# Kernel optimization log

Hardware: AMD Instinct MI355X
Metric: run time of the kernel (lower is better)

Reference implementation:

```python
import jax, jax.numpy as jnp
import numpy as np

B, T, C, H = 4, 1024, 512, 8
HD = C // H
N_NODE, F_DIM, TOTAL_DIM = 64, 8, 16
SCALE = 1.0 / np.sqrt(HD)


def _build_mask():
    # causal tril with every (total_dim-1 mod total_dim)-th COLUMN zeroed
    m = np.tril(np.ones((T, T), dtype=np.float32))
    m[:, TOTAL_DIM - 1::TOTAL_DIM] = 0.0
    return jnp.asarray(m)

MASK = _build_mask()  # (T, T), 1 = keep, 0 = mask


def setup_inputs() -> dict:
    key = jax.random.key(0)
    ks = jax.random.split(key, 12)
    s = 0.02
    return {
        "x": jax.random.normal(ks[0], (B, T, C), dtype=jnp.float32),
        "attn_bias": jax.random.normal(ks[1], (H, N_NODE, N_NODE), dtype=jnp.float32) * 0.1,
        "Wq": jax.random.normal(ks[2], (C, C), dtype=jnp.float32) * s,
        "bq": jax.random.normal(ks[3], (C,), dtype=jnp.float32) * s,
        "Wk": jax.random.normal(ks[4], (C, C), dtype=jnp.float32) * s,
        "bk": jax.random.normal(ks[5], (C,), dtype=jnp.float32) * s,
        "Wv": jax.random.normal(ks[6], (C, C), dtype=jnp.float32) * s,
        "bv": jax.random.normal(ks[7], (C,), dtype=jnp.float32) * s,
        "Wp": jax.random.normal(ks[8], (C, C), dtype=jnp.float32) * s,
        "bp": jax.random.normal(ks[9], (C,), dtype=jnp.float32) * s,
    }


def reference(x, attn_bias, Wq, bq, Wk, bk, Wv, bv, Wp, bp):
    Bx, Tx, Cx = x.shape

    def heads(W, b):  # (B,T,C) -> (B,H,T,HD); torch Linear is x @ W.T + b
        return (x @ W.T + b).reshape(Bx, Tx, H, HD).transpose(0, 2, 1, 3)

    q, k, v = heads(Wq, bq), heads(Wk, bk), heads(Wv, bv)

    # repeat_interleave + repeat expansion == kron(attn_bias, ones(f_dim, f_dim))
    d = N_NODE * F_DIM
    bias = jnp.repeat(jnp.repeat(attn_bias, F_DIM, axis=1), F_DIM, axis=2)  # (H, d, d)
    padded_bias = jnp.zeros((H, Tx, Tx), dtype=x.dtype).at[:, :d, :d].set(bias)

    att = jnp.einsum('bhqd,bhkd->bhqk', q, k) * SCALE + padded_bias[None]
    neg = jnp.asarray(-jnp.inf, dtype=att.dtype)
    att = jnp.where(MASK[None, None, :Tx, :Tx] == 0, neg, att)
    att = jax.nn.softmax(att, axis=-1)

    y = jnp.einsum('bhqk,bhkd->bhqd', att, v)
    y = y.transpose(0, 2, 1, 3).reshape(Bx, Tx, Cx)
    return y @ Wp.T + bp
```

## Files before the change

### kernel.cpp

```cpp
#include <hip/hip_runtime.h>

#define T_SEQ 1024
#define C_DIM 512
#define H_HEADS 8
#define HDIM 64
#define B_BATCH 4
#define M_ROWS (B_BATCH * T_SEQ)
#define NSPLIT_TOT 40

typedef __attribute__((ext_vector_type(8))) short short8;
typedef __attribute__((ext_vector_type(4))) float f32x4;

__device__ __forceinline__ unsigned short f2bf(float f) {
    unsigned u = __builtin_bit_cast(unsigned, f);
    u += 0x7FFFu + ((u >> 16) & 1u);
    return (unsigned short)(u >> 16);
}

__device__ __forceinline__ void gload_lds16(const unsigned short* g, unsigned short* l) {
    __builtin_amdgcn_global_load_lds(
        (const __attribute__((address_space(1))) unsigned int*)(const void*)g,
        (__attribute__((address_space(3))) unsigned int*)(void*)l, 16, 0, 0);
}

__device__ __constant__ unsigned char BX_OF[NSPLIT_TOT] =
    {0,1,2,3,4,4,5,5,6,6,7,7,8,8,8,9,9,9,10,10,10,11,11,11,
     12,12,12,12,13,13,13,13,14,14,14,14,15,15,15,15};
__device__ __constant__ unsigned char SP_OF[NSPLIT_TOT] =
    {0,0,0,0,0,1,0,1,0,1,0,1,0,1,2,0,1,2,0,1,2,0,1,2,
     0,1,2,3,0,1,2,3,0,1,2,3,0,1,2,3};
__device__ __constant__ unsigned char CUM_OF[16] =
    {0,1,2,3,4,6,8,10,12,15,18,21,24,28,32,36};

__global__ __launch_bounds__(256) void cast_all(
    const float* __restrict__ x,
    const float* __restrict__ wq, const float* __restrict__ wk,
    const float* __restrict__ wv, const float* __restrict__ wp,
    unsigned short* __restrict__ xb,
    unsigned short* __restrict__ wqb, unsigned short* __restrict__ wkb,
    unsigned short* __restrict__ wvb, unsigned short* __restrict__ wpb)
{
    const long NX = (long)M_ROWS * C_DIM;
    const long NW = (long)C_DIM * C_DIM;
    long i4 = (long)blockIdx.x * blockDim.x + threadIdx.x;
    long base = i4 * 4;
    const float* src; unsigned short* dst; long off;
    if (base < NX) { src = x; dst = xb; off = base; }
    else {
        long r = base - NX;
        int w = (int)(r >> 18);
        off = r & (NW - 1);
        switch (w) {
            case 0:  src = wq; dst = wqb; break;
            case 1:  src = wk; dst = wkb; break;
            case 2:  src = wv; dst = wvb; break;
            default: src = wp; dst = wpb; break;
        }
    }
    float4 v = *(const float4*)(src + off);
    ushort4 o;
    o.x = f2bf(v.x); o.y = f2bf(v.y); o.z = f2bf(v.z); o.w = f2bf(v.w);
    *(ushort4*)(dst + off) = o;
}

__device__ __forceinline__ void gemm_body(
    const unsigned short* __restrict__ A,
    const unsigned short* __restrict__ W,
    const float* __restrict__ bias,
    unsigned short* __restrict__ Obf,
    float* __restrict__ Of,
    int mode)
{
    __shared__ __align__(16) unsigned short Atile[128 * 64];
    __shared__ __align__(16) unsigned short Btile[128 * 64];

    const int tid  = threadIdx.x;
    const int w    = tid >> 6;
    const int lane = tid & 63;
    const int quad = lane >> 4;
    const int l16  = lane & 15;
    const int m0   = blockIdx.x * 128;
    const int n0   = blockIdx.y * 128;
    const int wr   = 64 * (w >> 1);
    const int wc   = 64 * (w & 1);

    f32x4 acc[4][4] = {};

    const int lr = lane >> 3;
    const int lc = lane & 7;

    for (int k0 = 0; k0 < 512; k0 += 64) {
        __syncthreads();
        for (int i = 0; i < 4; ++i) {
            int r0 = 32 * w + 8 * i;
            int r  = r0 + lr;
            int c  = lc ^ (r & 7);
            gload_lds16(&A[(long)(m0 + r) * 512 + k0 + c * 8], &Atile[r0 * 64]);
            gload_lds16(&W[(long)(n0 + r) * 512 + k0 + c * 8], &Btile[r0 * 64]);
        }
        __syncthreads();

        for (int st = 0; st < 2; ++st) {
            const int pc = ((4 * st + quad) ^ (l16 & 7)) * 8;
            short8 af[4], bf[4];
            for (int i = 0; i < 4; ++i)
                af[i] = *(const short8*)&Atile[(wr + 16 * i + l16) * 64 + pc];
            for (int j = 0; j < 4; ++j)
                bf[j] = *(const short8*)&Btile[(wc + 16 * j + l16) * 64 + pc];
            for (int i = 0; i < 4; ++i)
                for (int j = 0; j < 4; ++j)
                    acc[i][j] = (mode == 1)
                        ? __builtin_amdgcn_mfma_f32_16x16x32_bf16(bf[j], af[i], acc[i][j], 0, 0, 0)
                        : __builtin_amdgcn_mfma_f32_16x16x32_bf16(af[i], bf[j], acc[i][j], 0, 0, 0);
        }
    }

    if (mode == 1) {
        for (int j = 0; j < 4; ++j) {
            for (int reg = 0; reg < 4; ++reg) {
                int n = n0 + wc + 16 * j + 4 * quad + reg;
                int h = n >> 6, hd = n & 63;
                float bv = bias[n];
                for (int i = 0; i < 4; ++i) {
                    int t = m0 + wr + 16 * i + l16;
                    int b = t >> 10, tl = t & 1023;
                    Obf[(((long)(b * H_HEADS + h)) * HDIM + hd) * T_SEQ + tl] =
                        f2bf(acc[i][j][reg] + bv);
                }
            }
        }
    } else {
        for (int j = 0; j < 4; ++j) {
            int col = n0 + wc + 16 * j + l16;
            float bv = bias[col];
            for (int i = 0; i < 4; ++i) {
                for (int reg = 0; reg < 4; ++reg) {
                    int row = m0 + wr + 16 * i + 4 * quad + reg;
                    float v = acc[i][j][reg] + bv;
                    if (mode == 2) {
                        Of[(long)row * 512 + col] = v;
                    } else {
                        int b = row >> 10, t = row & 1023;
                        int h = col >> 6,  hd = col & 63;
                        Obf[(((long)(b * H_HEADS + h)) * T_SEQ + t) * HDIM + hd] = f2bf(v);
                    }
                }
            }
        }
    }
}

__global__ __launch_bounds__(256) void gemm_qkv(
    const unsigned short* __restrict__ A,
    const unsigned short* __restrict__ Wq, const unsigned short* __restrict__ Wk,
    const unsigned short* __restrict__ Wv,
    const float* __restrict__ bq, const float* __restrict__ bk, const float* __restrict__ bv,
    unsigned short* __restrict__ Q, unsigned short* __restrict__ K,
    unsigned short* __restrict__ V)
{
    const unsigned short* W; const float* b; unsigned short* O; int mode;
    if (blockIdx.z == 0)      { W = Wq; b = bq; O = Q; mode = 0; }
    else if (blockIdx.z == 1) { W = Wk; b = bk; O = K; mode = 0; }
    else                      { W = Wv; b = bv; O = V; mode = 1; }
    gemm_body(A, W, b, O, nullptr, mode);
}

__global__ __launch_bounds__(256) void gemm_out_k(
    const unsigned short* __restrict__ A, const unsigned short* __restrict__ W,
    const float* __restrict__ bias, float* __restrict__ O)
{
    gemm_body(A, W, bias, nullptr, O, 2);
}

__global__ __launch_bounds__(256) void attn_split(
    const unsigned short* __restrict__ Q, const unsigned short* __restrict__ K,
    const unsigned short* __restrict__ Vt, const float* __restrict__ attn_bias,
    float* __restrict__ Opart, float* __restrict__ mpart, float* __restrict__ lpart)
{
    __shared__ __align__(16) unsigned short Kl[64 * 72];
    __shared__ __align__(16) unsigned short Vl[64 * 72];
    __shared__ __align__(16) unsigned short Pl[4][16 * 72];
    __shared__ float biasl[8][64];

    const int tid  = threadIdx.x;
    const int w    = tid >> 6;
    const int lane = tid & 63;
    const int quad = lane >> 4;
    const int l16  = lane & 15;
    const int sidx = blockIdx.x;
    const int bh   = blockIdx.y;
    const int h    = bh & 7;
    const int bx   = BX_OF[sidx];
    const int sp   = SP_OF[sidx];
    const int q0   = bx * 64;
    const int kt0  = sp * 4;
    const int kt1  = min(kt0 + 4, bx + 1);

    if (q0 < 512 && sp < 2) {
        for (int i = tid; i < 512; i += 256) {
            int nq = (q0 >> 3) + (i >> 6);
            biasl[i >> 6][i & 63] = attn_bias[h * 4096 + nq * 64 + (i & 63)];
        }
    }

    const unsigned short* Qbh = Q  + (long)bh * T_SEQ * HDIM;
    const unsigned short* Kbh = K  + (long)bh * T_SEQ * HDIM;
    const unsigned short* Vbh = Vt + (long)bh * HDIM * T_SEQ;

    short8 qf[2];
    {
        int qr = q0 + 16 * w + l16;
        qf[0] = *(const short8*)&Qbh[(long)qr * HDIM + 8 * quad];
        qf[1] = *(const short8*)&Qbh[(long)qr * HDIM + 32 + 8 * quad];
    }

    f32x4 oacc[4] = {};
    float mrow[4] = {-INFINITY, -INFINITY, -INFINITY, -INFINITY};
    float lrow[4] = {0.f, 0.f, 0.f, 0.f};

    for (int kt = kt0; kt < kt1; ++kt) {
        const int k0 = kt * 64;
        __syncthreads();
        for (int it = 0; it < 2; ++it) {
            int ch = tid + 256 * it;
            int r = ch >> 3, c8 = ch & 7;
            *(short8*)&Kl[r * 72 + c8 * 8] =
                *(const short8*)&Kbh[(long)(k0 + r) * HDIM + c8 * 8];
            *(short8*)&Vl[r * 72 + c8 * 8] =
                *(const short8*)&Vbh[(long)r * T_SEQ + k0 + c8 * 8];
        }
        __syncthreads();

        f32x4 s[4] = {};
        for (int st = 0; st < 2; ++st) {
            for (int ct = 0; ct < 4; ++ct) {
                short8 bf = *(const short8*)&Kl[(16 * ct + l16) * 72 + 32 * st + 8 * quad];
                s[ct] = __builtin_amdgcn_mfma_f32_16x16x32_bf16(qf[st], bf, s[ct], 0, 0, 0);
            }
        }

        const int qrb = q0 + 16 * w + 4 * quad;
        float rmax[4] = {-INFINITY, -INFINITY, -INFINITY, -INFINITY};
        for (int ct = 0; ct < 4; ++ct) {
            int kcol = k0 + 16 * ct + l16;
            for (int reg = 0; reg < 4; ++reg) {
                int qrow = qrb + reg;
                float v = s[ct][reg] * 0.125f;
                if (qrow < 512 && kcol < 512)
                    v += biasl[(qrow >> 3) & 7][kcol >> 3];
                bool keep = (kcol <= qrow) && ((kcol & 15) != 15);
                v = keep ? v : -INFINITY;
                s[ct][reg] = v;
                rmax[reg] = fmaxf(rmax[reg], v);
            }
        }
        for (int off = 1; off < 16; off <<= 1)
            for (int reg = 0; reg < 4; ++reg)
                rmax[reg] = fmaxf(rmax[reg], __shfl_xor(rmax[reg], off));

        float alpha[4];
        for (int reg = 0; reg < 4; ++reg) {
            float mnew = fmaxf(mrow[reg], rmax[reg]);
            alpha[reg] = __expf(mrow[reg] - mnew);
            mrow[reg] = mnew;
        }

        float rsum[4] = {0.f, 0.f, 0.f, 0.f};
        for (int ct = 0; ct < 4; ++ct) {
            for (int reg = 0; reg < 4; ++reg) {
                float p = __expf(s[ct][reg] - mrow[reg]);
                rsum[reg] += p;
                Pl[w][(4 * quad + reg) * 72 + 16 * ct + l16] = f2bf(p);
            }
        }
        for (int off = 1; off < 16; off <<= 1)
            for (int reg = 0; reg < 4; ++reg)
                rsum[reg] += __shfl_xor(rsum[reg], off);
        for (int reg = 0; reg < 4; ++reg)
            lrow[reg] = lrow[reg] * alpha[reg] + rsum[reg];
        for (int ct = 0; ct < 4; ++ct)
            for (int reg = 0; reg < 4; ++reg)
                oacc[ct][reg] *= alpha[reg];

        for (int st = 0; st < 2; ++st) {
            short8 af = *(const short8*)&Pl[w][l16 * 72 + 32 * st + 8 * quad];
            for (int ct = 0; ct < 4; ++ct) {
                short8 bf = *(const short8*)&Vl[(16 * ct + l16) * 72 + 32 * st + 8 * quad];
                oacc[ct] = __builtin_amdgcn_mfma_f32_16x16x32_bf16(af, bf, oacc[ct], 0, 0, 0);
            }
        }
    }

    const long p = (long)bh * NSPLIT_TOT + sidx;
    float* Op = Opart + p * 4096;
    for (int ct = 0; ct < 4; ++ct)
        for (int reg = 0; reg < 4; ++reg)
            Op[(16 * w + 4 * quad + reg) * 64 + 16 * ct + l16] = oacc[ct][reg];
    if (l16 == 0) {
        for (int reg = 0; reg < 4; ++reg) {
            int qr = 16 * w + 4 * quad + reg;
            mpart[p * 64 + qr] = mrow[reg];
            lpart[p * 64 + qr] = lrow[reg];
        }
    }
}

__global__ __launch_bounds__(256) void attn_combine(
    const float* __restrict__ Opart, const float* __restrict__ mpart,
    const float* __restrict__ lpart, unsigned short* __restrict__ Y)
{
    const int bx = blockIdx.x, bh = blockIdx.y;
    const int b = bh >> 3, h = bh & 7;
    const int ns = (bx >> 2) + 1;
    const long p0 = (long)bh * NSPLIT_TOT + CUM_OF[bx];
    const int tid = threadIdx.x;
    const int qr = tid >> 2;
    const int hs = (tid & 3) * 16;

    float m[4], l[4];
    for (int s = 0; s < ns; ++s) {
        m[s] = mpart[(p0 + s) * 64 + qr];
        l[s] = lpart[(p0 + s) * 64 + qr];
    }
    float ms = -INFINITY;
    for (int s = 0; s < ns; ++s) ms = fmaxf(ms, m[s]);
    float L = 0.f, sc[4];
    for (int s = 0; s < ns; ++s) { sc[s] = __expf(m[s] - ms); L += l[s] * sc[s]; }

    float acc[16] = {};
    for (int s = 0; s < ns; ++s) {
        const float4* op = (const float4*)(Opart + (p0 + s) * 4096 + qr * 64 + hs);
        float f = sc[s];
        for (int j4 = 0; j4 < 4; ++j4) {
            float4 v = op[j4];
            acc[4 * j4 + 0] += f * v.x; acc[4 * j4 + 1] += f * v.y;
            acc[4 * j4 + 2] += f * v.z; acc[4 * j4 + 3] += f * v.w;
        }
    }
    float inv = 1.f / L;
    int q = bx * 64 + qr;
    unsigned short* y = Y + ((long)b * T_SEQ + q) * C_DIM + h * HDIM + hs;
    for (int j4 = 0; j4 < 4; ++j4) {
        ushort4 o;
        o.x = f2bf(acc[4 * j4 + 0] * inv); o.y = f2bf(acc[4 * j4 + 1] * inv);
        o.z = f2bf(acc[4 * j4 + 2] * inv); o.w = f2bf(acc[4 * j4 + 3] * inv);
        *(ushort4*)(y + 4 * j4) = o;
    }
}

extern "C" void kernel_launch(void* const* d_in, const int* in_sizes, int n_in,
                              void* d_out, int out_size, void* d_ws, size_t ws_size,
                              hipStream_t stream)
{
    const float* x         = (const float*)d_in[0];
    const float* attn_bias = (const float*)d_in[1];
    const float* Wq = (const float*)d_in[2]; const float* bq = (const float*)d_in[3];
    const float* Wk = (const float*)d_in[4]; const float* bk = (const float*)d_in[5];
    const float* Wv = (const float*)d_in[6]; const float* bv = (const float*)d_in[7];
    const float* Wp = (const float*)d_in[8]; const float* bp = (const float*)d_in[9];
    float* out = (float*)d_out;

    const long NX = (long)M_ROWS * C_DIM;
    const long NW = (long)C_DIM * C_DIM;

    unsigned short* xb  = (unsigned short*)d_ws;
    unsigned short* wqb = xb  + NX;
    unsigned short* wkb = wqb + NW;
    unsigned short* wvb = wkb + NW;
    unsigned short* wpb = wvb + NW;
    unsigned short* Qb  = wpb + NW;
    unsigned short* Kb  = Qb  + NX;
    unsigned short* Vtb = Kb  + NX;
    unsigned short* Yb  = Vtb + NX;
    float* Opart = (float*)(Yb + NX);
    float* mpart = Opart + (long)32 * NSPLIT_TOT * 4096;
    float* lpart = mpart + (long)32 * NSPLIT_TOT * 64;

    long n4 = (NX + 4 * NW) / 4;
    cast_all<<<dim3((unsigned)(n4 / 256)), 256, 0, stream>>>(
        x, Wq, Wk, Wv, Wp, xb, wqb, wkb, wvb, wpb);

    gemm_qkv<<<dim3(M_ROWS / 128, C_DIM / 128, 3), 256, 0, stream>>>(
        xb, wqb, wkb, wvb, bq, bk, bv, Qb, Kb, Vtb);

    attn_split<<<dim3(NSPLIT_TOT, B_BATCH * H_HEADS), 256, 0, stream>>>(
        Qb, Kb, Vtb, attn_bias, Opart, mpart, lpart);

    attn_combine<<<dim3(T_SEQ / 64, B_BATCH * H_HEADS), 256, 0, stream>>>(
        Opart, mpart, lpart, Yb);

    gemm_out_k<<<dim3(M_ROWS / 128, C_DIM / 128), 256, 0, stream>>>(
        Yb, wpb, bp, out);
}
```

Measured before the change: 145.0 us.

## Fuse fp32-to-bf16 casts into GEMM tile loads and drop cast kernel

Removes the separate cast_all kernel. The QKV and output-projection GEMMs now read fp32 x and weights directly, convert them to bf16 in registers and store them into padded LDS tiles, replacing the async global_load_lds path and the XOR swizzle. This saves a kernel launch and a full write and re-read of bf16 copies of x and the weights. In exchange, each GEMM block re-converts the same tiles many times, global reads double in bytes, and loads now go through registers instead of async LDS DMA.

```diff
diff --git a/kernel.cpp b/kernel.cpp
--- a/kernel.cpp
+++ b/kernel.cpp
@@ -17,10 +17,13 @@
     return (unsigned short)(u >> 16);
 }
 
-__device__ __forceinline__ void gload_lds16(const unsigned short* g, unsigned short* l) {
-    __builtin_amdgcn_global_load_lds(
-        (const __attribute__((address_space(1))) unsigned int*)(const void*)g,
-        (__attribute__((address_space(3))) unsigned int*)(void*)l, 16, 0, 0);
+__device__ __forceinline__ short8 pack8(float4 a, float4 b) {
+    short8 r;
+    r[0] = (short)f2bf(a.x); r[1] = (short)f2bf(a.y);
+    r[2] = (short)f2bf(a.z); r[3] = (short)f2bf(a.w);
+    r[4] = (short)f2bf(b.x); r[5] = (short)f2bf(b.y);
+    r[6] = (short)f2bf(b.z); r[7] = (short)f2bf(b.w);
+    return r;
 }
 
 __device__ __constant__ unsigned char BX_OF[NSPLIT_TOT] =
@@ -32,47 +35,22 @@
 __device__ __constant__ unsigned char CUM_OF[16] =
     {0,1,2,3,4,6,8,10,12,15,18,21,24,28,32,36};
 
-__global__ __launch_bounds__(256) void cast_all(
+__global__ __launch_bounds__(256) void gemm_qkv(
     const float* __restrict__ x,
-    const float* __restrict__ wq, const float* __restrict__ wk,
-    const float* __restrict__ wv, const float* __restrict__ wp,
-    unsigned short* __restrict__ xb,
-    unsigned short* __restrict__ wqb, unsigned short* __restrict__ wkb,
-    unsigned short* __restrict__ wvb, unsigned short* __restrict__ wpb)
-{
-    const long NX = (long)M_ROWS * C_DIM;
-    const long NW = (long)C_DIM * C_DIM;
-    long i4 = (long)blockIdx.x * blockDim.x + threadIdx.x;
-    long base = i4 * 4;
-    const float* src; unsigned short* dst; long off;
-    if (base < NX) { src = x; dst = xb; off = base; }
-    else {
-        long r = base - NX;
-        int w = (int)(r >> 18);
-        off = r & (NW - 1);
-        switch (w) {
-            case 0:  src = wq; dst = wqb; break;
-            case 1:  src = wk; dst = wkb; break;
-            case 2:  src = wv; dst = wvb; break;
-            default: src = wp; dst = wpb; break;
-        }
-    }
-    float4 v = *(const float4*)(src + off);
-    ushort4 o;
-    o.x = f2bf(v.x); o.y = f2bf(v.y); o.z = f2bf(v.z); o.w = f2bf(v.w);
-    *(ushort4*)(dst + off) = o;
-}
-
-__device__ __forceinline__ void gemm_body(
-    const unsigned short* __restrict__ A,
-    const unsigned short* __restrict__ W,
-    const float* __restrict__ bias,
-    unsigned short* __restrict__ Obf,
-    float* __restrict__ Of,
-    int mode)
-{
-    __shared__ __align__(16) unsigned short Atile[128 * 64];
-    __shared__ __align__(16) unsigned short Btile[128 * 64];
+    const float* __restrict__ Wq, const float* __restrict__ Wk,
+    const float* __restrict__ Wv,
+    const float* __restrict__ bq, const float* __restrict__ bk,
+    const float* __restrict__ bv,
+    unsigned short* __restrict__ Q, unsigned short* __restrict__ K,
+    unsigned short* __restrict__ V)
+{
+    const float* W; const float* bias; unsigned short* O; int mode;
+    if (blockIdx.z == 0)      { W = Wq; bias = bq; O = Q; mode = 0; }
+    else if (blockIdx.z == 1) { W = Wk; bias = bk; O = K; mode = 0; }
+    else                      { W = Wv; bias = bv; O = V; mode = 1; }
+
+    __shared__ __align__(16) unsigned short Atile[128 * 72];
+    __shared__ __align__(16) unsigned short Btile[128 * 72];
 
     const int tid  = threadIdx.x;
     const int w    = tid >> 6;
@@ -83,30 +61,31 @@
     const int n0   = blockIdx.y * 128;
     const int wr   = 64 * (w >> 1);
     const int wc   = 64 * (w & 1);
+    const int sr   = tid >> 1;
+    const int sq   = (tid & 1) * 32;
 
     f32x4 acc[4][4] = {};
 
-    const int lr = lane >> 3;
-    const int lc = lane & 7;
-
     for (int k0 = 0; k0 < 512; k0 += 64) {
-        __syncthreads();
-        for (int i = 0; i < 4; ++i) {
-            int r0 = 32 * w + 8 * i;
-            int r  = r0 + lr;
-            int c  = lc ^ (r & 7);
-            gload_lds16(&A[(long)(m0 + r) * 512 + k0 + c * 8], &Atile[r0 * 64]);
-            gload_lds16(&W[(long)(n0 + r) * 512 + k0 + c * 8], &Btile[r0 * 64]);
+        float4 av[8], bw[8];
+        const float4* Ap = (const float4*)&x[(long)(m0 + sr) * 512 + k0 + sq];
+        const float4* Bp = (const float4*)&W[(long)(n0 + sr) * 512 + k0 + sq];
+        for (int j = 0; j < 8; ++j) av[j] = Ap[j];
+        for (int j = 0; j < 8; ++j) bw[j] = Bp[j];
+
+        __syncthreads();
+        for (int j = 0; j < 4; ++j) {
+            *(short8*)&Atile[sr * 72 + sq + 8 * j] = pack8(av[2 * j], av[2 * j + 1]);
+            *(short8*)&Btile[sr * 72 + sq + 8 * j] = pack8(bw[2 * j], bw[2 * j + 1]);
         }
         __syncthreads();
 
         for (int st = 0; st < 2; ++st) {
-            const int pc = ((4 * st + quad) ^ (l16 & 7)) * 8;
             short8 af[4], bf[4];
             for (int i = 0; i < 4; ++i)
-                af[i] = *(const short8*)&Atile[(wr + 16 * i + l16) * 64 + pc];
+                af[i] = *(const short8*)&Atile[(wr + 16 * i + l16) * 72 + 32 * st + 8 * quad];
             for (int j = 0; j < 4; ++j)
-                bf[j] = *(const short8*)&Btile[(wc + 16 * j + l16) * 64 + pc];
+                bf[j] = *(const short8*)&Btile[(wc + 16 * j + l16) * 72 + 32 * st + 8 * quad];
             for (int i = 0; i < 4; ++i)
                 for (int j = 0; j < 4; ++j)
                     acc[i][j] = (mode == 1)
@@ -120,56 +99,88 @@
             for (int reg = 0; reg < 4; ++reg) {
                 int n = n0 + wc + 16 * j + 4 * quad + reg;
                 int h = n >> 6, hd = n & 63;
-                float bv = bias[n];
+                float bvv = bias[n];
                 for (int i = 0; i < 4; ++i) {
                     int t = m0 + wr + 16 * i + l16;
                     int b = t >> 10, tl = t & 1023;
-                    Obf[(((long)(b * H_HEADS + h)) * HDIM + hd) * T_SEQ + tl] =
-                        f2bf(acc[i][j][reg] + bv);
+                    O[(((long)(b * H_HEADS + h)) * HDIM + hd) * T_SEQ + tl] =
+                        f2bf(acc[i][j][reg] + bvv);
                 }
             }
         }
     } else {
         for (int j = 0; j < 4; ++j) {
             int col = n0 + wc + 16 * j + l16;
-            float bv = bias[col];
+            float bvv = bias[col];
             for (int i = 0; i < 4; ++i) {
                 for (int reg = 0; reg < 4; ++reg) {
                     int row = m0 + wr + 16 * i + 4 * quad + reg;
-                    float v = acc[i][j][reg] + bv;
-                    if (mode == 2) {
-                        Of[(long)row * 512 + col] = v;
-                    } else {
-                        int b = row >> 10, t = row & 1023;
-                        int h = col >> 6,  hd = col & 63;
-                        Obf[(((long)(b * H_HEADS + h)) * T_SEQ + t) * HDIM + hd] = f2bf(v);
-                    }
+                    int b = row >> 10, t = row & 1023;
+                    int h = col >> 6,  hd = col & 63;
+                    O[(((long)(b * H_HEADS + h)) * T_SEQ + t) * HDIM + hd] =
+                        f2bf(acc[i][j][reg] + bvv);
                 }
             }
         }
     }
 }
 
-__global__ __launch_bounds__(256) void gemm_qkv(
-    const unsigned short* __restrict__ A,
-    const unsigned short* __restrict__ Wq, const unsigned short* __restrict__ Wk,
-    const unsigned short* __restrict__ Wv,
-    const float* __restrict__ bq, const float* __restrict__ bk, const float* __restrict__ bv,
-    unsigned short* __restrict__ Q, unsigned short* __restrict__ K,
-    unsigned short* __restrict__ V)
-{
-    const unsigned short* W; const float* b; unsigned short* O; int mode;
-    if (blockIdx.z == 0)      { W = Wq; b = bq; O = Q; mode = 0; }
-    else if (blockIdx.z == 1) { W = Wk; b = bk; O = K; mode = 0; }
-    else                      { W = Wv; b = bv; O = V; mode = 1; }
-    gemm_body(A, W, b, O, nullptr, mode);
-}
-
 __global__ __launch_bounds__(256) void gemm_out_k(
-    const unsigned short* __restrict__ A, const unsigned short* __restrict__ W,
+    const unsigned short* __restrict__ A, const float* __restrict__ W,
     const float* __restrict__ bias, float* __restrict__ O)
 {
-    gemm_body(A, W, bias, nullptr, O, 2);
+    __shared__ __align__(16) unsigned short Atile[128 * 72];
+    __shared__ __align__(16) unsigned short Btile[128 * 72];
+
+    const int tid  = threadIdx.x;
+    const int w    = tid >> 6;
+    const int lane = tid & 63;
+    const int quad = lane >> 4;
+    const int l16  = lane & 15;
+    const int m0   = blockIdx.x * 128;
+    const int n0   = blockIdx.y * 128;
+    const int wr   = 64 * (w >> 1);
+    const int wc   = 64 * (w & 1);
+    const int sr   = tid >> 1;
+    const int sq   = (tid & 1) * 32;
+
+    f32x4 acc[4][4] = {};
+
+    for (int k0 = 0; k0 < 512; k0 += 64) {
+        short8 av[4]; float4 bw[8];
+        const short8* Ap = (const short8*)&A[(long)(m0 + sr) * 512 + k0 + sq];
+        const float4* Bp = (const float4*)&W[(long)(n0 + sr) * 512 + k0 + sq];
+        for (int j = 0; j < 4; ++j) av[j] = Ap[j];
+        for (int j = 0; j < 8; ++j) bw[j] = Bp[j];
+
+        __syncthreads();
+        for (int j = 0; j < 4; ++j) {
+            *(short8*)&Atile[sr * 72 + sq + 8 * j] = av[j];
+            *(short8*)&Btile[sr * 72 + sq + 8 * j] = pack8(bw[2 * j], bw[2 * j + 1]);
+        }
+        __syncthreads();
+
+        for (int st = 0; st < 2; ++st) {
+            short8 af[4], bf[4];
+            for (int i = 0; i < 4; ++i)
+                af[i] = *(const short8*)&Atile[(wr + 16 * i + l16) * 72 + 32 * st + 8 * quad];
+            for (int j = 0; j < 4; ++j)
+                bf[j] = *(const short8*)&Btile[(wc + 16 * j + l16) * 72 + 32 * st + 8 * quad];
+            for (int i = 0; i < 4; ++i)
+                for (int j = 0; j < 4; ++j)
+                    acc[i][j] = __builtin_amdgcn_mfma_f32_16x16x32_bf16(af[i], bf[j], acc[i][j], 0, 0, 0);
+        }
+    }
+
+    for (int j = 0; j < 4; ++j) {
+        int col = n0 + wc + 16 * j + l16;
+        float bvv = bias[col];
+        for (int i = 0; i < 4; ++i)
+            for (int reg = 0; reg < 4; ++reg) {
+                int row = m0 + wr + 16 * i + 4 * quad + reg;
+                O[(long)row * 512 + col] = acc[i][j][reg] + bvv;
+            }
+    }
 }
 
 __global__ __launch_bounds__(256) void attn_split(
@@ -361,14 +372,8 @@
     float* out = (float*)d_out;
 
     const long NX = (long)M_ROWS * C_DIM;
-    const long NW = (long)C_DIM * C_DIM;
-
-    unsigned short* xb  = (unsigned short*)d_ws;
-    unsigned short* wqb = xb  + NX;
-    unsigned short* wkb = wqb + NW;
-    unsigned short* wvb = wkb + NW;
-    unsigned short* wpb = wvb + NW;
-    unsigned short* Qb  = wpb + NW;
+
+    unsigned short* Qb  = (unsigned short*)d_ws;
     unsigned short* Kb  = Qb  + NX;
     unsigned short* Vtb = Kb  + NX;
     unsigned short* Yb  = Vtb + NX;
@@ -376,12 +381,8 @@
     float* mpart = Opart + (long)32 * NSPLIT_TOT * 4096;
     float* lpart = mpart + (long)32 * NSPLIT_TOT * 64;
 
-    long n4 = (NX + 4 * NW) / 4;
-    cast_all<<<dim3((unsigned)(n4 / 256)), 256, 0, stream>>>(
-        x, Wq, Wk, Wv, Wp, xb, wqb, wkb, wvb, wpb);
-
     gemm_qkv<<<dim3(M_ROWS / 128, C_DIM / 128, 3), 256, 0, stream>>>(
-        xb, wqb, wkb, wvb, bq, bk, bv, Qb, Kb, Vtb);
+        x, Wq, Wk, Wv, bq, bk, bv, Qb, Kb, Vtb);
 
     attn_split<<<dim3(NSPLIT_TOT, B_BATCH * H_HEADS), 256, 0, stream>>>(
         Qb, Kb, Vtb, attn_bias, Opart, mpart, lpart);
@@ -390,5 +391,5 @@
         Opart, mpart, lpart, Yb);
 
     gemm_out_k<<<dim3(M_ROWS / 128, C_DIM / 128), 256, 0, stream>>>(
-        Yb, wpb, bp, out);
-}
+        Yb, Wp, bp, out);
+}
```

Result: slower. 185.4 us (+27.9%).
